# Kernel optimization log

Hardware: AMD Instinct MI355X
Metric: run time of the kernel (lower is better)

## Reference

```python
import jax, jax.numpy as jnp
import numpy as np

N = 208   # number of nodes (hard-coded ring graph in source)
K = 4     # k-hop receptive field

def _support(n=N, k=K):
    # ring adjacency: node i connected to i-1 and i+1 (wrap-around)
    A = np.zeros((n, n), dtype=np.float64)
    idx = np.arange(n)
    A[idx, (idx + 1) % n] = 1.0
    A[idx, (idx - 1) % n] = 1.0
    # normalized_laplacian in source: adj + diag(1/deg)
    L = A + np.diag(1.0 / A.sum(axis=1))
    # calculate_adjacency_k: sign(L^k) -> band mask of width 2k+1
    Lk = np.linalg.matrix_power(L, k)
    return np.sign(Lk).astype(np.float32)


def setup_inputs() -> dict:
    key = jax.random.key(0)
    k1, k2 = jax.random.split(key)
    B, T = 64, 2048
    x = jax.random.normal(k1, (B, T, N), dtype=jnp.float32)
    # per-node non-shared kernel [N, N], glorot-ish scale
    W = jax.random.normal(k2, (N, N), dtype=jnp.float32) * (1.0 / np.sqrt(N))
    b = jnp.zeros((N,), dtype=jnp.float32)
    S = jnp.asarray(_support())  # fixed k-hop adjacency mask
    return {"x": x, "W": W, "b": b, "S": S}


def reference(x, W, b, S):
    # Locally-connected GC: mask the [N,N] kernel by the k-hop support,
    # then apply as a node-mixing linear transform per (batch, time).
    out = jnp.einsum('btn,nm->btm', x, S * W) + b
    return out  # activation=None in init
```

## Files before the change

### kernel.cpp

```cpp
#include <hip/hip_runtime.h>


#define NN   208
#define NC   52
#define HW   4
#define BAND 9
#define TR   16
#define THREADS 832
#define NBLK 512
#define TILE_F  (TR * NN)
#define DEPTH 4

typedef float vfloat4 __attribute__((ext_vector_type(4)));

__global__ __launch_bounds__(THREADS) void lcgc_kernel(
    const float* __restrict__ x,
    const float* __restrict__ W,
    const float* __restrict__ b,
    const float* __restrict__ S,
    float* __restrict__ out,
    int total_rows)
{
    __shared__ float sX[DEPTH][TILE_F];
    __shared__ float sBand[BAND * NN];

    const int tid = threadIdx.x;

    for (int i = tid; i < BAND * NN; i += THREADS) {
        int d = i / NN;
        int m = i - d * NN;
        int n = m + d - HW;
        if (n < 0) n += NN;
        else if (n >= NN) n -= NN;
        sBand[i] = W[n * NN + m] * S[n * NN + m];
    }
    __syncthreads();

    const int c    = tid % NC;
    const int rg   = tid / NC;
    const int wave = tid >> 6;

    const float4 bias4 = *reinterpret_cast<const float4*>(&b[c * 4]);
    const int cm = (c == 0)      ? NC - 1 : c - 1;
    const int cp = (c == NC - 1) ? 0      : c + 1;

    const long long ntiles_total = total_rows / TR;
    const long long nt = ntiles_total / gridDim.x;
    const long long t0 = (long long)blockIdx.x * nt;

    float* const ldsw = &sX[0][wave * 256];

    #define STAGE(kt)                                                         \
        do {                                                                  \
            const float* gsrc = x + (t0 + (kt)) * TILE_F + (long long)tid * 4;\
            float* ldst = ldsw + (int)((kt) & (DEPTH - 1)) * TILE_F;          \
            __builtin_amdgcn_global_load_lds(                                 \
                (const __attribute__((address_space(1))) void*)(gsrc),        \
                (__attribute__((address_space(3))) void*)(ldst),              \
                16, 0, 0);                                                    \
        } while (0)

    #define COMPUTE(kt)                                                       \
        do {                                                                  \
            const float4* xr4 = reinterpret_cast<const float4*>(              \
                &sX[(int)((kt) & (DEPTH - 1))][rg * NN]);                     \
            const float4 a = xr4[cm];                                         \
            const float4 m4 = xr4[c];                                         \
            const float4 e = xr4[cp];                                         \
            const float xv[12] = {a.x, a.y, a.z, a.w,                         \
                                  m4.x, m4.y, m4.z, m4.w,                     \
                                  e.x, e.y, e.z, e.w};                        \
            float4 acc = bias4;                                               \
            const float4* band4 = reinterpret_cast<const float4*>(sBand);     \
            _Pragma("unroll")                                                 \
            for (int d = 0; d < BAND; ++d) {                                  \
                const float4 bd = band4[d * NC + c];                          \
                acc.x = fmaf(bd.x, xv[0 + d], acc.x);                         \
                acc.y = fmaf(bd.y, xv[1 + d], acc.y);                         \
                acc.z = fmaf(bd.z, xv[2 + d], acc.z);                         \
                acc.w = fmaf(bd.w, xv[3 + d], acc.w);                         \
            }                                                                 \
            vfloat4 av = {acc.x, acc.y, acc.z, acc.w};                        \
            __builtin_nontemporal_store(av, reinterpret_cast<vfloat4*>(       \
                out + (t0 + (kt)) * TILE_F + rg * NN + c * 4));               \
        } while (0)

    STAGE(0); STAGE(1); STAGE(2);

    for (long long k = 0; k < nt; ++k) {
        if (k + 3 < nt) STAGE(k + 3);
        {
            const int a1 = (int)(k < 3 ? k : 3);
            const int a2 = (int)((nt - 1 - k) < 3 ? (nt - 1 - k) : 3);
            switch (a1 + a2) {
            case 0: asm volatile("s_waitcnt vmcnt(0)" ::: "memory"); break;
            case 1: asm volatile("s_waitcnt vmcnt(1)" ::: "memory"); break;
            case 2: asm volatile("s_waitcnt vmcnt(2)" ::: "memory"); break;
            case 3: asm volatile("s_waitcnt vmcnt(3)" ::: "memory"); break;
            case 4: asm volatile("s_waitcnt vmcnt(4)" ::: "memory"); break;
            case 5: asm volatile("s_waitcnt vmcnt(5)" ::: "memory"); break;
            default: asm volatile("s_waitcnt vmcnt(6)" ::: "memory"); break;
            }
        }
        __builtin_amdgcn_sched_barrier(0);
        __builtin_amdgcn_s_barrier();
        COMPUTE(k);
        asm volatile("" ::: "memory");
        __builtin_amdgcn_s_barrier();
    }

    #undef STAGE
    #undef COMPUTE
}

extern "C" void kernel_launch(void* const* d_in, const int* in_sizes, int n_in,
                              void* d_out, int out_size, void* d_ws, size_t ws_size,
                              hipStream_t stream) {
    const float* x = (const float*)d_in[0];
    const float* W = (const float*)d_in[1];
    const float* b = (const float*)d_in[2];
    const float* S = (const float*)d_in[3];
    float* out = (float*)d_out;

    const int total_rows = in_sizes[0] / NN;
    lcgc_kernel<<<dim3(NBLK), dim3(THREADS), 0, stream>>>(
        x, W, b, S, out, total_rows);
}
```

Baseline: 51.66 us.

## Double tile rows per stage and switch to two-deep LDS double buffering

Each tile now holds 32 rows, loaded with two async global-to-LDS loads per thread. Every thread computes two output rows per iteration, so the barrier and wait overhead is spread over twice the data. Pipelining drops from four buffers with three tiles in flight to two buffers with one tile in flight, which keeps LDS usage about the same but reduces how much load latency is hidden. Bias is now read from shared memory, and the vmcnt waits are adjusted to count stores as well as loads.

```diff
diff --git a/kernel.cpp b/kernel.cpp
--- a/kernel.cpp
+++ b/kernel.cpp
@@ -5,11 +5,11 @@
 #define NC   52
 #define HW   4
 #define BAND 9
-#define TR   16
+#define TR   32
 #define THREADS 832
 #define NBLK 512
 #define TILE_F  (TR * NN)
-#define DEPTH 4
+#define TILE_F4 (TILE_F / 4)
 
 typedef float vfloat4 __attribute__((ext_vector_type(4)));
 
@@ -21,8 +21,9 @@
     float* __restrict__ out,
     int total_rows)
 {
-    __shared__ float sX[DEPTH][TILE_F];
+    __shared__ float sX[2][TILE_F];
     __shared__ float sBand[BAND * NN];
+    __shared__ float sBias[NN];
 
     const int tid = threadIdx.x;
 
@@ -34,13 +35,13 @@
         else if (n >= NN) n -= NN;
         sBand[i] = W[n * NN + m] * S[n * NN + m];
     }
+    if (tid < NN) sBias[tid] = b[tid];
     __syncthreads();
 
     const int c    = tid % NC;
     const int rg   = tid / NC;
     const int wave = tid >> 6;
 
-    const float4 bias4 = *reinterpret_cast<const float4*>(&b[c * 4]);
     const int cm = (c == 0)      ? NC - 1 : c - 1;
     const int cp = (c == NC - 1) ? 0      : c + 1;
 
@@ -48,30 +49,33 @@
     const long long nt = ntiles_total / gridDim.x;
     const long long t0 = (long long)blockIdx.x * nt;
 
-    float* const ldsw = &sX[0][wave * 256];
+    float* const ldswA = &sX[0][wave * 256];
+    float* const ldswB = &sX[0][3328 + wave * 256];
 
     #define STAGE(kt)                                                         \
         do {                                                                  \
-            const float* gsrc = x + (t0 + (kt)) * TILE_F + (long long)tid * 4;\
-            float* ldst = ldsw + (int)((kt) & (DEPTH - 1)) * TILE_F;          \
+            const long long base = (t0 + (kt)) * TILE_F;                      \
+            const int bo = (int)((kt) & 1) * TILE_F;                          \
             __builtin_amdgcn_global_load_lds(                                 \
-                (const __attribute__((address_space(1))) void*)(gsrc),        \
-                (__attribute__((address_space(3))) void*)(ldst),              \
+                (const __attribute__((address_space(1))) void*)               \
+                    (x + base + (long long)tid * 4),                          \
+                (__attribute__((address_space(3))) void*)(ldswA + bo),        \
+                16, 0, 0);                                                    \
+            __builtin_amdgcn_global_load_lds(                                 \
+                (const __attribute__((address_space(1))) void*)               \
+                    (x + base + 3328 + (long long)tid * 4),                   \
+                (__attribute__((address_space(3))) void*)(ldswB + bo),        \
                 16, 0, 0);                                                    \
         } while (0)
 
-    #define COMPUTE(kt)                                                       \
+    #define ROWCOMP(xr4, acc)                                                 \
         do {                                                                  \
-            const float4* xr4 = reinterpret_cast<const float4*>(              \
-                &sX[(int)((kt) & (DEPTH - 1))][rg * NN]);                     \
-            const float4 a = xr4[cm];                                         \
-            const float4 m4 = xr4[c];                                         \
-            const float4 e = xr4[cp];                                         \
+            const float4 a = (xr4)[cm];                                       \
+            const float4 m4 = (xr4)[c];                                       \
+            const float4 e = (xr4)[cp];                                       \
             const float xv[12] = {a.x, a.y, a.z, a.w,                         \
                                   m4.x, m4.y, m4.z, m4.w,                     \
                                   e.x, e.y, e.z, e.w};                        \
-            float4 acc = bias4;                                               \
-            const float4* band4 = reinterpret_cast<const float4*>(sBand);     \
             _Pragma("unroll")                                                 \
             for (int d = 0; d < BAND; ++d) {                                  \
                 const float4 bd = band4[d * NC + c];                          \
@@ -80,26 +84,41 @@
                 acc.z = fmaf(bd.z, xv[2 + d], acc.z);                         \
                 acc.w = fmaf(bd.w, xv[3 + d], acc.w);                         \
             }                                                                 \
-            vfloat4 av = {acc.x, acc.y, acc.z, acc.w};                        \
-            __builtin_nontemporal_store(av, reinterpret_cast<vfloat4*>(       \
-                out + (t0 + (kt)) * TILE_F + rg * NN + c * 4));               \
         } while (0)
 
-    STAGE(0); STAGE(1); STAGE(2);
+    #define COMPUTE(kt)                                                       \
+        do {                                                                  \
+            const int bi = (int)((kt) & 1);                                   \
+            const float4* band4 = reinterpret_cast<const float4*>(sBand);     \
+            const float4 bias4 =                                              \
+                *reinterpret_cast<const float4*>(&sBias[c * 4]);              \
+            const float4* xr4a =                                              \
+                reinterpret_cast<const float4*>(&sX[bi][rg * NN]);            \
+            const float4* xr4b =                                              \
+                reinterpret_cast<const float4*>(&sX[bi][(rg + 16) * NN]);     \
+            float4 acc0 = bias4;                                              \
+            float4 acc1 = bias4;                                              \
+            ROWCOMP(xr4a, acc0);                                              \
+            ROWCOMP(xr4b, acc1);                                              \
+            const long long grow = (t0 + (kt)) * TR + rg;                     \
+            vfloat4 av0 = {acc0.x, acc0.y, acc0.z, acc0.w};                   \
+            vfloat4 av1 = {acc1.x, acc1.y, acc1.z, acc1.w};                   \
+            __builtin_nontemporal_store(av0, reinterpret_cast<vfloat4*>(      \
+                out + grow * NN + c * 4));                                    \
+            __builtin_nontemporal_store(av1, reinterpret_cast<vfloat4*>(      \
+                out + (grow + 16) * NN + c * 4));                             \
+        } while (0)
+
+    STAGE(0);
 
     for (long long k = 0; k < nt; ++k) {
-        if (k + 3 < nt) STAGE(k + 3);
+        if (k + 1 < nt) STAGE(k + 1);
         {
-            const int a1 = (int)(k < 3 ? k : 3);
-            const int a2 = (int)((nt - 1 - k) < 3 ? (nt - 1 - k) : 3);
-            switch (a1 + a2) {
+            const int nv = (k >= 1 ? 2 : 0) + (k + 1 < nt ? 2 : 0);
+            switch (nv) {
             case 0: asm volatile("s_waitcnt vmcnt(0)" ::: "memory"); break;
-            case 1: asm volatile("s_waitcnt vmcnt(1)" ::: "memory"); break;
             case 2: asm volatile("s_waitcnt vmcnt(2)" ::: "memory"); break;
-            case 3: asm volatile("s_waitcnt vmcnt(3)" ::: "memory"); break;
-            case 4: asm volatile("s_waitcnt vmcnt(4)" ::: "memory"); break;
-            case 5: asm volatile("s_waitcnt vmcnt(5)" ::: "memory"); break;
-            default: asm volatile("s_waitcnt vmcnt(6)" ::: "memory"); break;
+            default: asm volatile("s_waitcnt vmcnt(4)" ::: "memory"); break;
             }
         }
         __builtin_amdgcn_sched_barrier(0);
@@ -110,6 +129,7 @@
     }
 
     #undef STAGE
+    #undef ROWCOMP
     #undef COMPUTE
 }
 
```

Measured after the change: 45.24 us. 1.14x faster.
